# Performance work log

Measured on AMD Instinct MI355X. Metric: run time of the kernel, lower is better.

Reference implementation:

```python
import jax, jax.numpy as jnp
import numpy as np

B, S, D = 2, 2048, 1024
M = 2048          # d_mlp
E = 8             # num_experts
TOP_K = 2


def setup_inputs() -> dict:
    key = jax.random.key(0)
    ks = jax.random.split(key, 5)
    std = 0.02
    return {
        "residual": jax.random.normal(ks[0], (B, S, D), jnp.float32),
        "W_router": jax.random.normal(ks[1], (D, E), jnp.float32) * std,
        "W_gate": jax.random.normal(ks[2], (E, D, M), jnp.float32) * std,
        "b_gate": jnp.zeros((E, M), jnp.float32),
        "W_up": jax.random.normal(ks[3], (E, D, M), jnp.float32) * std,
        "b_up": jnp.zeros((E, M), jnp.float32),
        "W_out": jax.random.normal(ks[4], (E, M, D), jnp.float32) * std,
        "b_out": jnp.zeros((E, D), jnp.float32),
    }


def reference(residual, W_router, W_gate, b_gate, W_up, b_up, W_out, b_out):
    # --- router: softmax over experts, top-k selection, renormalize ---
    router_logits = jnp.einsum('bsd,de->bse', residual, W_router)
    router_probs = jax.nn.softmax(router_logits, axis=-1)
    top_k_probs, top_k_idx = jax.lax.top_k(router_probs, TOP_K)          # [B,S,K]
    top_k_probs = top_k_probs / (jnp.sum(top_k_probs, -1, keepdims=True) + 1e-8)
    # per-expert combine weight [B,S,E]; top-k indices are unique per token
    one_hot = jax.nn.one_hot(top_k_idx, E, dtype=residual.dtype)          # [B,S,K,E]
    expert_weights = jnp.einsum('bsk,bske->bse', top_k_probs, one_hot)
    # --- each expert runs dense SwiGLU MLP on the FULL batch (compute-then-mask, as in source) ---
    gate = jax.nn.silu(jnp.einsum('bsd,edm->ebsm', residual, W_gate) + b_gate[:, None, None, :])
    up = jnp.einsum('bsd,edm->ebsm', residual, W_up) + b_up[:, None, None, :]
    hidden = gate * up                                                    # [E,B,S,M]
    expert_out = jnp.einsum('ebsm,emd->ebsd', hidden, W_out) + b_out[:, None, None, :]
    # --- weighted combine (weights are zero for non-selected experts) ---
    output = jnp.einsum('bse,ebsd->bsd', expert_weights, expert_out)
    return output
```

## Files before the change

kernel.cpp:

```cpp
#include <hip/hip_runtime.h>
#include <cstdint>
#include <cstddef>

#define TT 4096
#define DD 1024
#define MM 2048
#define EE 8
#define NPAIR 8192

typedef unsigned short u16;
typedef __bf16 bf16x8 __attribute__((ext_vector_type(8)));
typedef float f32x4 __attribute__((ext_vector_type(4)));
typedef u16 u16x8 __attribute__((ext_vector_type(8)));
typedef __attribute__((address_space(3))) void* lds_vp;
typedef __attribute__((address_space(1))) const void* gbl_cvp;

__device__ __forceinline__ void async16(u16* l, const u16* g) {
  __builtin_amdgcn_global_load_lds((gbl_cvp)(const void*)g, (lds_vp)(void*)l, 16, 0, 0);
}

#define VMCNT6() asm volatile("s_waitcnt vmcnt(6)" ::: "memory")
#define VMCNT4() asm volatile("s_waitcnt vmcnt(4)" ::: "memory")
#define VMCNT0() asm volatile("s_waitcnt vmcnt(0)" ::: "memory")
#define BARR() do { asm volatile("" ::: "memory"); __builtin_amdgcn_s_barrier(); asm volatile("" ::: "memory"); } while (0)

__device__ __forceinline__ u16 f2bf(float f) {
  uint32_t u = __builtin_bit_cast(uint32_t, f);
  u += 0x7fffu + ((u >> 16) & 1u);
  return (u16)(u >> 16);
}
__device__ __forceinline__ float bf2f(u16 h) {
  uint32_t u = ((uint32_t)h) << 16;
  return __builtin_bit_cast(float, u);
}

__global__ __launch_bounds__(256)
void prep_kernel(const float* __restrict__ X, const float* __restrict__ Wr,
                 int* __restrict__ tok_idx, float* __restrict__ wpair,
                 u16* __restrict__ Xbf,
                 const float* __restrict__ Gf, const float* __restrict__ Uf,
                 const float* __restrict__ Of, u16* __restrict__ tG,
                 u16* __restrict__ tU, u16* __restrict__ tO) {
  __shared__ float tile[64][65];
  int bid = blockIdx.x;
  if (bid < TT / 4) {
    int wave = threadIdx.x >> 6;
    int lane = threadIdx.x & 63;
    int t = bid * 4 + wave;
    const float4* x4 = (const float4*)(X + (size_t)t * DD);
    float acc[EE];
#pragma unroll
    for (int e = 0; e < EE; e++) acc[e] = 0.f;
#pragma unroll
    for (int i = 0; i < 4; i++) {
      float4 xv = x4[i * 64 + lane];
      ushort4 o;
      o.x = f2bf(xv.x); o.y = f2bf(xv.y); o.z = f2bf(xv.z); o.w = f2bf(xv.w);
      *(ushort4*)&Xbf[(size_t)t * DD + (size_t)(i * 64 + lane) * 4] = o;
      const float4* wr4 = (const float4*)(Wr + (size_t)(i * 256 + lane * 4) * EE);
      float xs[4] = {xv.x, xv.y, xv.z, xv.w};
#pragma unroll
      for (int c = 0; c < 4; c++) {
        float4 wa = wr4[c * 2 + 0];
        float4 wb = wr4[c * 2 + 1];
        acc[0] += xs[c] * wa.x; acc[1] += xs[c] * wa.y;
        acc[2] += xs[c] * wa.z; acc[3] += xs[c] * wa.w;
        acc[4] += xs[c] * wb.x; acc[5] += xs[c] * wb.y;
        acc[6] += xs[c] * wb.z; acc[7] += xs[c] * wb.w;
      }
    }
#pragma unroll
    for (int off = 32; off > 0; off >>= 1)
#pragma unroll
      for (int e = 0; e < EE; e++) acc[e] += __shfl_xor(acc[e], off);
    if (lane == 0) {
      float mx = acc[0];
#pragma unroll
      for (int e = 1; e < EE; e++) mx = fmaxf(mx, acc[e]);
      float p[EE], s = 0.f;
#pragma unroll
      for (int e = 0; e < EE; e++) { p[e] = __expf(acc[e] - mx); s += p[e]; }
      float inv = 1.f / s;
#pragma unroll
      for (int e = 0; e < EE; e++) p[e] *= inv;
      int i0 = 0;
#pragma unroll
      for (int e = 1; e < EE; e++) if (p[e] > p[i0]) i0 = e;
      int i1 = (i0 == 0) ? 1 : 0;
#pragma unroll
      for (int e = 0; e < EE; e++) if (e != i0 && p[e] > p[i1]) i1 = e;
      float denom = p[i0] + p[i1] + 1e-8f;
      tok_idx[t * 2 + 0] = i0;
      tok_idx[t * 2 + 1] = i1;
      wpair[t * 2 + 0] = p[i0] / denom;
      wpair[t * 2 + 1] = p[i1] / denom;
    }
    return;
  }
  int idx = bid - TT / 4;
  int z = idx >> 9;
  int tidx = idx & 511;
  const float* in; u16* out; int R, C, shift, e;
  if (z < 8)       { in = Gf; out = tG; R = DD; C = MM; e = z;      shift = 5; }
  else if (z < 16) { in = Uf; out = tU; R = DD; C = MM; e = z - 8;  shift = 5; }
  else             { in = Of; out = tO; R = MM; C = DD; e = z - 16; shift = 4; }
  int cx = tidx & ((1 << shift) - 1);
  int cy = tidx >> shift;
  const float* I = in + (size_t)e * R * C;
  u16* O = out + (size_t)e * R * C;
  int c0 = cx * 64, r0 = cy * 64;
  int t = threadIdx.x;
  {
    int cq = t & 15;
    int rb = t >> 4;
#pragma unroll
    for (int i = 0; i < 4; i++) {
      int r = rb + i * 16;
      float4 v = *(const float4*)&I[(size_t)(r0 + r) * C + c0 + cq * 4];
      tile[cq * 4 + 0][r] = v.x;
      tile[cq * 4 + 1][r] = v.y;
      tile[cq * 4 + 2][r] = v.z;
      tile[cq * 4 + 3][r] = v.w;
    }
  }
  __syncthreads();
  {
    int rseg = (t & 7) * 8;
    int cc = t >> 3;
#pragma unroll
    for (int i = 0; i < 2; i++) {
      int c = cc + i * 32;
      u16x8 o;
#pragma unroll
      for (int k = 0; k < 8; k++) o[k] = f2bf(tile[c][rseg + k]);
      *(u16x8*)&O[(size_t)(c0 + c) * R + r0 + rseg] = o;
    }
  }
}

__global__ void bucket_kernel(const int* __restrict__ tok_idx, int* __restrict__ offsets,
                              int* __restrict__ bucket) {
  __shared__ int lcnt[EE];
  __shared__ int lcur[EE];
  int tid = threadIdx.x;
  int lane = tid & 63;
  if (tid < EE) lcnt[tid] = 0;
  __syncthreads();
  {
    int cnt[EE];
#pragma unroll
    for (int k = 0; k < EE; k++) cnt[k] = 0;
    for (int i = tid; i < NPAIR; i += 1024) {
      int e = tok_idx[i];
#pragma unroll
      for (int k = 0; k < EE; k++) {
        unsigned long long m = __ballot(e == k);
        cnt[k] += __popcll(m);
      }
    }
    if (lane == 0) {
#pragma unroll
      for (int k = 0; k < EE; k++)
        if (cnt[k]) atomicAdd(&lcnt[k], cnt[k]);
    }
  }
  __syncthreads();
  if (tid == 0) {
    int s = 0;
    for (int e = 0; e < EE; e++) {
      offsets[e] = s;
      lcur[e] = s;
      s += lcnt[e];
    }
    offsets[EE] = s;
  }
  __syncthreads();
  for (int i = tid; i < NPAIR; i += 1024) {
    int e = tok_idx[i];
    int pos = 0;
#pragma unroll
    for (int k = 0; k < EE; k++) {
      unsigned long long m = __ballot(e == k);
      int c = __popcll(m);
      if (c) {
        int leader = (int)__ffsll((long long)m) - 1;
        int base = 0;
        if (lane == leader) base = atomicAdd(&lcur[k], c);
        base = __shfl(base, leader);
        if (e == k) pos = base + __popcll(m & ((1ull << lane) - 1ull));
      }
    }
    bucket[pos] = i;
  }
}

__device__ __forceinline__ bool tile_map(const int* __restrict__ offsets, int x,
                                         int& expert, int& row0, int& rows) {
  expert = -1;
#pragma unroll 1
  for (int e = 0; e < EE; e++) {
    int o0 = offsets[e], o1 = offsets[e + 1];
    int nt = (o1 - o0 + 127) >> 7;
    if (x < nt) { expert = e; row0 = o0 + (x << 7); rows = min(128, o1 - row0); return true; }
    x -= nt;
  }
  return false;
}

__device__ __forceinline__ void grid_decode(int bid, int& rt, int& n0) {
  int xcd = bid & 7, slot = bid >> 3;
  rt = xcd * 9 + slot % 9;
  n0 = (slot / 9) * 128;
}


__global__ __launch_bounds__(256, 2)
void moe_gemm_gu(const u16* __restrict__ Xbf, const u16* __restrict__ WtG,
                 const u16* __restrict__ WtU, const float* __restrict__ bgate,
                 const float* __restrict__ bup, u16* __restrict__ Hws,
                 const int* __restrict__ offsets, const int* __restrict__ bucket) {
  int rt, n0;
  grid_decode(blockIdx.x, rt, n0);
  int expert, row0, rows;
  if (!tile_map(offsets, rt, expert, row0, rows)) return;

  __shared__ u16 Alds[3 * 128 * 32];
  __shared__ u16 Glds[3 * 128 * 32];
  __shared__ u16 Ulds[3 * 128 * 32];

  int tid = threadIdx.x;
  int wave = tid >> 6, lane = tid & 63;
  int wm = wave >> 1, wn = wave & 1;
  int quad = lane >> 4, l15 = lane & 15;
  int swz = ((lane & 3) ^ ((lane >> 3) & 3)) * 8;
  int rp  = (quad ^ ((l15 >> 1) & 3)) * 8;

  long arow0, arow1;
  {
    int r0l = wave * 32 + (lane >> 2);
    int rr0 = min(r0l, rows - 1);
    int rr1 = min(r0l + 16, rows - 1);
    arow0 = (long)(bucket[row0 + rr0] >> 1) * DD;
    arow1 = (long)(bucket[row0 + rr1] >> 1) * DD;
  }
  const u16* A0 = Xbf + arow0 + swz;
  const u16* A1 = Xbf + arow1 + swz;
  size_t bo = (size_t)expert * MM * DD + (size_t)n0 * DD
            + (long)(wave * 32 + (lane >> 2)) * DD + swz;
  const u16* G0 = WtG + bo; const u16* G1 = G0 + 16 * DD;
  const u16* U0 = WtU + bo; const u16* U1 = U0 + 16 * DD;

  int sb0 = (wave * 32) * 32, sb1 = (wave * 32 + 16) * 32;

  f32x4 accG[4][4], accU[4][4];
#pragma unroll
  for (int i = 0; i < 4; i++)
#pragma unroll
    for (int j = 0; j < 4; j++) { accG[i][j] = (f32x4){0,0,0,0}; accU[i][j] = (f32x4){0,0,0,0}; }

  auto stage = [&](int b) {
    int bo2 = b * (128 * 32);
    async16(&Alds[bo2 + sb0], A0); async16(&Alds[bo2 + sb1], A1);
    async16(&Glds[bo2 + sb0], G0); async16(&Glds[bo2 + sb1], G1);
    async16(&Ulds[bo2 + sb0], U0); async16(&Ulds[bo2 + sb1], U1);
    A0 += 32; A1 += 32; G0 += 32; G1 += 32; U0 += 32; U1 += 32;
  };

  auto compute = [&](int b) {
    int ro = b * (128 * 32);
    bf16x8 af[4], bg[4], bu[4];
#pragma unroll
    for (int i = 0; i < 4; i++) {
      af[i] = *(const bf16x8*)&Alds[ro + (wm * 64 + i * 16 + l15) * 32 + rp];
      bg[i] = *(const bf16x8*)&Glds[ro + (wn * 64 + i * 16 + l15) * 32 + rp];
      bu[i] = *(const bf16x8*)&Ulds[ro + (wn * 64 + i * 16 + l15) * 32 + rp];
    }
    __builtin_amdgcn_s_setprio(1);
#pragma unroll
    for (int i = 0; i < 4; i++)
#pragma unroll
      for (int j = 0; j < 4; j++)
        accG[i][j] = __builtin_amdgcn_mfma_f32_16x16x32_bf16(af[i], bg[j], accG[i][j], 0, 0, 0);
#pragma unroll
    for (int i = 0; i < 4; i++)
#pragma unroll
      for (int j = 0; j < 4; j++)
        accU[i][j] = __builtin_amdgcn_mfma_f32_16x16x32_bf16(af[i], bu[j], accU[i][j], 0, 0, 0);
    __builtin_amdgcn_s_setprio(0);
  };

  constexpr int NT = DD / 32;
  stage(0);
  stage(1);
  int br = 0, bs = 2;
#pragma unroll 3
  for (int t = 0; t < NT - 2; ++t) {
    VMCNT6();
    BARR();
    stage(bs);
    compute(br);
    bs = br; br = (br + 1 == 3) ? 0 : br + 1;
  }
  VMCNT6(); BARR(); compute(br); br = (br + 1 == 3) ? 0 : br + 1;
  VMCNT0(); BARR(); compute(br);

#pragma unroll
  for (int i = 0; i < 4; i++) {
    int lrb = wm * 64 + i * 16 + quad * 4;
#pragma unroll
    for (int j = 0; j < 4; j++) {
      int gc = n0 + wn * 64 + j * 16 + l15;
      float bgv = bgate[expert * MM + gc];
      float buv = bup[expert * MM + gc];
#pragma unroll
      for (int r = 0; r < 4; r++) {
        int lr = lrb + r;
        if (lr < rows) {
          int grow = row0 + lr;
          float g = accG[i][j][r] + bgv;
          float u = accU[i][j][r] + buv;
          float sg = g / (1.f + __expf(-g));
          Hws[(size_t)grow * MM + gc] = f2bf(sg * u);
        }
      }
    }
  }
}

__global__ __launch_bounds__(256, 3)
void moe_gemm_out(const u16* __restrict__ Hmat, const u16* __restrict__ WtO,
                  const float* __restrict__ bias, float* __restrict__ Ypart,
                  const int* __restrict__ offsets, const int* __restrict__ bucket,
                  const float* __restrict__ wpair) {
  int rt, n0;
  grid_decode(blockIdx.x, rt, n0);
  int expert, row0, rows;
  if (!tile_map(offsets, rt, expert, row0, rows)) return;

  __shared__ u16 Alds[3 * 128 * 32];
  __shared__ u16 Blds[3 * 128 * 32];

  int tid = threadIdx.x;
  int wave = tid >> 6, lane = tid & 63;
  int wm = wave >> 1, wn = wave & 1;
  int quad = lane >> 4, l15 = lane & 15;
  int swz = ((lane & 3) ^ ((lane >> 3) & 3)) * 8;
  int rp  = (quad ^ ((l15 >> 1) & 3)) * 8;

  long arow0, arow1;
  {
    int r0l = wave * 32 + (lane >> 2);
    int rr0 = min(r0l, rows - 1);
    int rr1 = min(r0l + 16, rows - 1);
    arow0 = (long)(row0 + rr0) * MM;
    arow1 = (long)(row0 + rr1) * MM;
  }
  const u16* A0 = Hmat + arow0 + swz;
  const u16* A1 = Hmat + arow1 + swz;
  const u16* B0 = WtO + (size_t)expert * DD * MM + (size_t)n0 * MM
                + (long)(wave * 32 + (lane >> 2)) * MM + swz;
  const u16* B1 = B0 + 16 * MM;

  int sb0 = (wave * 32) * 32, sb1 = (wave * 32 + 16) * 32;

  f32x4 acc[4][4];
#pragma unroll
  for (int i = 0; i < 4; i++)
#pragma unroll
    for (int j = 0; j < 4; j++) acc[i][j] = (f32x4){0, 0, 0, 0};

  auto stage = [&](int b) {
    int bo2 = b * (128 * 32);
    async16(&Alds[bo2 + sb0], A0); async16(&Alds[bo2 + sb1], A1);
    async16(&Blds[bo2 + sb0], B0); async16(&Blds[bo2 + sb1], B1);
    A0 += 32; A1 += 32; B0 += 32; B1 += 32;
  };

  auto compute = [&](int b) {
    int ro = b * (128 * 32);
    bf16x8 af[4], bf[4];
#pragma unroll
    for (int i = 0; i < 4; i++) {
      af[i] = *(const bf16x8*)&Alds[ro + (wm * 64 + i * 16 + l15) * 32 + rp];
      bf[i] = *(const bf16x8*)&Blds[ro + (wn * 64 + i * 16 + l15) * 32 + rp];
    }
    __builtin_amdgcn_s_setprio(1);
#pragma unroll
    for (int i = 0; i < 4; i++)
#pragma unroll
      for (int j = 0; j < 4; j++)
        acc[i][j] = __builtin_amdgcn_mfma_f32_16x16x32_bf16(af[i], bf[j], acc[i][j], 0, 0, 0);
    __builtin_amdgcn_s_setprio(0);
  };

  constexpr int NT = MM / 32;
  stage(0);
  stage(1);
  int br = 0, bs = 2;
#pragma unroll 2
  for (int t = 0; t < NT - 2; ++t) {
    VMCNT4();
    BARR();
    stage(bs);
    compute(br);
    bs = br; br = (br + 1 == 3) ? 0 : br + 1;
  }
  VMCNT4(); BARR(); compute(br); br = (br + 1 == 3) ? 0 : br + 1;
  VMCNT0(); BARR(); compute(br);

#pragma unroll
  for (int i = 0; i < 4; i++) {
    int lrb = wm * 64 + i * 16 + quad * 4;
#pragma unroll
    for (int j = 0; j < 4; j++) {
      int gc = n0 + wn * 64 + j * 16 + l15;
      float bv = bias[expert * DD + gc];
#pragma unroll
      for (int r = 0; r < 4; r++) {
        int lr = lrb + r;
        if (lr < rows) {
          int grow = row0 + lr;
          int p = bucket[grow];
          float w = wpair[p];
          Ypart[(size_t)p * DD + gc] = w * (acc[i][j][r] + bv);
        }
      }
    }
  }
}

__global__ void combine_kernel(const float* __restrict__ Ypart, float* __restrict__ out) {
  int i = blockIdx.x * 256 + threadIdx.x;
  int t = i >> 8;
  int c4 = i & 255;
  const float4* y0 = (const float4*)(Ypart + (size_t)(2 * t) * DD) + c4;
  const float4* y1 = (const float4*)(Ypart + (size_t)(2 * t + 1) * DD) + c4;
  float4 a = *y0, b = *y1;
  float4 o;
  o.x = a.x + b.x; o.y = a.y + b.y; o.z = a.z + b.z; o.w = a.w + b.w;
  ((float4*)out)[i] = o;
}

extern "C" void kernel_launch(void* const* d_in, const int* in_sizes, int n_in,
                              void* d_out, int out_size, void* d_ws, size_t ws_size,
                              hipStream_t stream) {
  const float* residual = (const float*)d_in[0];
  const float* W_router = (const float*)d_in[1];
  const float* W_gate   = (const float*)d_in[2];
  const float* b_gate   = (const float*)d_in[3];
  const float* W_up     = (const float*)d_in[4];
  const float* b_up     = (const float*)d_in[5];
  const float* W_out    = (const float*)d_in[6];
  const float* b_out    = (const float*)d_in[7];
  float* out = (float*)d_out;

  char* ws = (char*)d_ws;
  int*   tok_idx = (int*)(ws + 0);
  float* wpair   = (float*)(ws + 32768);
  int*   offsets = (int*)(ws + 65536);
  int*   bucket  = (int*)(ws + 65536 + 512);
  u16*   Xbf  = (u16*)(ws + 131072);
  u16*   WtG  = Xbf + (size_t)TT * DD;
  u16*   WtU  = WtG + (size_t)EE * MM * DD;
  u16*   WtO  = WtU + (size_t)EE * MM * DD;
  u16*   Hws  = WtO + (size_t)EE * DD * MM;
  float* Ypart = (float*)(Hws + (size_t)NPAIR * MM);

  prep_kernel<<<dim3(TT / 4 + 24 * 512), dim3(256), 0, stream>>>(
      residual, W_router, tok_idx, wpair, Xbf, W_gate, W_up, W_out, WtG, WtU, WtO);
  bucket_kernel<<<dim3(1), dim3(1024), 0, stream>>>(tok_idx, offsets, bucket);
  moe_gemm_gu<<<dim3(8 * 9 * 16), dim3(256), 0, stream>>>(Xbf, WtG, WtU, b_gate, b_up, Hws, offsets, bucket);
  moe_gemm_out<<<dim3(8 * 9 * 8), dim3(256), 0, stream>>>(Hws, WtO, b_out, Ypart, offsets, bucket, wpair);
  combine_kernel<<<dim3(TT * DD / 4 / 256), dim3(256), 0, stream>>>(Ypart, out);
}
```

Measured before the change: 447.0 us.

## Load A operand directly into registers, bypassing LDS, in both MoE GEMMs

In the gate/up and output GEMMs, the activation (A) tile is no longer staged through LDS with async global-to-LDS copies. Each wave now loads its own A fragments straight from global memory into double-buffered registers, one K-step ahead, and only the weight tiles stay in the triple-buffered LDS ring. This cuts LDS footprint and LDS read/write traffic for A. In exchange, the two waves sharing a row block each fetch the same A data from global memory, global latency for A is hidden by only one step of register prefetch, and register pressure rises.

```diff
diff --git a/kernel.cpp b/kernel.cpp
--- a/kernel.cpp
+++ b/kernel.cpp
@@ -19,8 +19,8 @@
   __builtin_amdgcn_global_load_lds((gbl_cvp)(const void*)g, (lds_vp)(void*)l, 16, 0, 0);
 }
 
-#define VMCNT6() asm volatile("s_waitcnt vmcnt(6)" ::: "memory")
 #define VMCNT4() asm volatile("s_waitcnt vmcnt(4)" ::: "memory")
+#define VMCNT2() asm volatile("s_waitcnt vmcnt(2)" ::: "memory")
 #define VMCNT0() asm volatile("s_waitcnt vmcnt(0)" ::: "memory")
 #define BARR() do { asm volatile("" ::: "memory"); __builtin_amdgcn_s_barrier(); asm volatile("" ::: "memory"); } while (0)
 
@@ -224,7 +224,6 @@
   int expert, row0, rows;
   if (!tile_map(offsets, rt, expert, row0, rows)) return;
 
-  __shared__ u16 Alds[3 * 128 * 32];
   __shared__ u16 Glds[3 * 128 * 32];
   __shared__ u16 Ulds[3 * 128 * 32];
 
@@ -235,16 +234,13 @@
   int swz = ((lane & 3) ^ ((lane >> 3) & 3)) * 8;
   int rp  = (quad ^ ((l15 >> 1) & 3)) * 8;
 
-  long arow0, arow1;
-  {
-    int r0l = wave * 32 + (lane >> 2);
-    int rr0 = min(r0l, rows - 1);
-    int rr1 = min(r0l + 16, rows - 1);
-    arow0 = (long)(bucket[row0 + rr0] >> 1) * DD;
-    arow1 = (long)(bucket[row0 + rr1] >> 1) * DD;
-  }
-  const u16* A0 = Xbf + arow0 + swz;
-  const u16* A1 = Xbf + arow1 + swz;
+  const u16* Ap[4];
+#pragma unroll
+  for (int i = 0; i < 4; i++) {
+    int r = min(wm * 64 + i * 16 + l15, rows - 1);
+    Ap[i] = Xbf + (size_t)(bucket[row0 + r] >> 1) * DD + quad * 8;
+  }
+
   size_t bo = (size_t)expert * MM * DD + (size_t)n0 * DD
             + (long)(wave * 32 + (lane >> 2)) * DD + swz;
   const u16* G0 = WtG + bo; const u16* G1 = G0 + 16 * DD;
@@ -258,20 +254,23 @@
 #pragma unroll
     for (int j = 0; j < 4; j++) { accG[i][j] = (f32x4){0,0,0,0}; accU[i][j] = (f32x4){0,0,0,0}; }
 
+  bf16x8 aA[4], aB[4];
+
+  auto aload = [&](bf16x8 (&d)[4], int t) {
+#pragma unroll
+    for (int i = 0; i < 4; i++) d[i] = *(const bf16x8*)(Ap[i] + t * 32);
+  };
   auto stage = [&](int b) {
-    int bo2 = b * (128 * 32);
-    async16(&Alds[bo2 + sb0], A0); async16(&Alds[bo2 + sb1], A1);
-    async16(&Glds[bo2 + sb0], G0); async16(&Glds[bo2 + sb1], G1);
-    async16(&Ulds[bo2 + sb0], U0); async16(&Ulds[bo2 + sb1], U1);
-    A0 += 32; A1 += 32; G0 += 32; G1 += 32; U0 += 32; U1 += 32;
-  };
-
-  auto compute = [&](int b) {
+    int o = b * (128 * 32);
+    async16(&Glds[o + sb0], G0); async16(&Glds[o + sb1], G1);
+    async16(&Ulds[o + sb0], U0); async16(&Ulds[o + sb1], U1);
+    G0 += 32; G1 += 32; U0 += 32; U1 += 32;
+  };
+  auto compute = [&](int b, const bf16x8 (&af)[4]) {
     int ro = b * (128 * 32);
-    bf16x8 af[4], bg[4], bu[4];
+    bf16x8 bg[4], bu[4];
 #pragma unroll
     for (int i = 0; i < 4; i++) {
-      af[i] = *(const bf16x8*)&Alds[ro + (wm * 64 + i * 16 + l15) * 32 + rp];
       bg[i] = *(const bf16x8*)&Glds[ro + (wn * 64 + i * 16 + l15) * 32 + rp];
       bu[i] = *(const bf16x8*)&Ulds[ro + (wn * 64 + i * 16 + l15) * 32 + rp];
     }
@@ -289,20 +288,22 @@
     __builtin_amdgcn_s_setprio(0);
   };
 
-  constexpr int NT = DD / 32;
-  stage(0);
-  stage(1);
-  int br = 0, bs = 2;
-#pragma unroll 3
-  for (int t = 0; t < NT - 2; ++t) {
-    VMCNT6();
-    BARR();
-    stage(bs);
-    compute(br);
-    bs = br; br = (br + 1 == 3) ? 0 : br + 1;
-  }
-  VMCNT6(); BARR(); compute(br); br = (br + 1 == 3) ? 0 : br + 1;
-  VMCNT0(); BARR(); compute(br);
+  stage(0); aload(aA, 0); stage(1);
+  int cb = 0;
+#pragma unroll 1
+  for (int t = 0; t < 30; t += 2) {
+    VMCNT4(); BARR();
+    aload(aB, t + 1);
+    stage((cb + 2) % 3);
+    compute(cb, aA);
+    VMCNT4(); BARR();
+    aload(aA, t + 2);
+    stage(cb);
+    compute((cb + 1) % 3, aB);
+    cb = (cb + 2) % 3;
+  }
+  VMCNT4(); BARR(); aload(aB, 31); compute(cb, aA);
+  VMCNT0(); BARR(); compute((cb + 1) % 3, aB);
 
 #pragma unroll
   for (int i = 0; i < 4; i++) {
@@ -337,7 +338,6 @@
   int expert, row0, rows;
   if (!tile_map(offsets, rt, expert, row0, rows)) return;
 
-  __shared__ u16 Alds[3 * 128 * 32];
   __shared__ u16 Blds[3 * 128 * 32];
 
   int tid = threadIdx.x;
@@ -347,16 +347,13 @@
   int swz = ((lane & 3) ^ ((lane >> 3) & 3)) * 8;
   int rp  = (quad ^ ((l15 >> 1) & 3)) * 8;
 
-  long arow0, arow1;
-  {
-    int r0l = wave * 32 + (lane >> 2);
-    int rr0 = min(r0l, rows - 1);
-    int rr1 = min(r0l + 16, rows - 1);
-    arow0 = (long)(row0 + rr0) * MM;
-    arow1 = (long)(row0 + rr1) * MM;
-  }
-  const u16* A0 = Hmat + arow0 + swz;
-  const u16* A1 = Hmat + arow1 + swz;
+  const u16* Ap[4];
+#pragma unroll
+  for (int i = 0; i < 4; i++) {
+    int r = min(wm * 64 + i * 16 + l15, rows - 1);
+    Ap[i] = Hmat + (size_t)(row0 + r) * MM + quad * 8;
+  }
+
   const u16* B0 = WtO + (size_t)expert * DD * MM + (size_t)n0 * MM
                 + (long)(wave * 32 + (lane >> 2)) * MM + swz;
   const u16* B1 = B0 + 16 * MM;
@@ -369,21 +366,23 @@
 #pragma unroll
     for (int j = 0; j < 4; j++) acc[i][j] = (f32x4){0, 0, 0, 0};
 
+  bf16x8 aA[4], aB[4];
+
+  auto aload = [&](bf16x8 (&d)[4], int t) {
+#pragma unroll
+    for (int i = 0; i < 4; i++) d[i] = *(const bf16x8*)(Ap[i] + t * 32);
+  };
   auto stage = [&](int b) {
-    int bo2 = b * (128 * 32);
-    async16(&Alds[bo2 + sb0], A0); async16(&Alds[bo2 + sb1], A1);
-    async16(&Blds[bo2 + sb0], B0); async16(&Blds[bo2 + sb1], B1);
-    A0 += 32; A1 += 32; B0 += 32; B1 += 32;
-  };
-
-  auto compute = [&](int b) {
+    int o = b * (128 * 32);
+    async16(&Blds[o + sb0], B0); async16(&Blds[o + sb1], B1);
+    B0 += 32; B1 += 32;
+  };
+  auto compute = [&](int b, const bf16x8 (&af)[4]) {
     int ro = b * (128 * 32);
-    bf16x8 af[4], bf[4];
-#pragma unroll
-    for (int i = 0; i < 4; i++) {
-      af[i] = *(const bf16x8*)&Alds[ro + (wm * 64 + i * 16 + l15) * 32 + rp];
+    bf16x8 bf[4];
+#pragma unroll
+    for (int i = 0; i < 4; i++)
       bf[i] = *(const bf16x8*)&Blds[ro + (wn * 64 + i * 16 + l15) * 32 + rp];
-    }
     __builtin_amdgcn_s_setprio(1);
 #pragma unroll
     for (int i = 0; i < 4; i++)
@@ -393,20 +392,22 @@
     __builtin_amdgcn_s_setprio(0);
   };
 
-  constexpr int NT = MM / 32;
-  stage(0);
-  stage(1);
-  int br = 0, bs = 2;
-#pragma unroll 2
-  for (int t = 0; t < NT - 2; ++t) {
-    VMCNT4();
-    BARR();
-    stage(bs);
-    compute(br);
-    bs = br; br = (br + 1 == 3) ? 0 : br + 1;
-  }
-  VMCNT4(); BARR(); compute(br); br = (br + 1 == 3) ? 0 : br + 1;
-  VMCNT0(); BARR(); compute(br);
+  stage(0); aload(aA, 0); stage(1);
+  int cb = 0;
+#pragma unroll 1
+  for (int t = 0; t < 62; t += 2) {
+    VMCNT2(); BARR();
+    aload(aB, t + 1);
+    stage((cb + 2) % 3);
+    compute(cb, aA);
+    VMCNT2(); BARR();
+    aload(aA, t + 2);
+    stage(cb);
+    compute((cb + 1) % 3, aB);
+    cb = (cb + 2) % 3;
+  }
+  VMCNT2(); BARR(); aload(aB, 63); compute(cb, aA);
+  VMCNT0(); BARR(); compute((cb + 1) % 3, aB);
 
 #pragma unroll
   for (int i = 0; i < 4; i++) {
```

Result: slower. 535.8 us (+19.9%).
